# Performance work log

Measured on AMD Instinct MI355X. Metric: run time of the kernel, lower is better.

The kernel has to match this reference:

```python
import jax, jax.numpy as jnp
import numpy as np

B = 32768      # batch
D = 2          # input_dim
H = 2048       # hidden_dim
NQ = 4         # qubits


def setup_inputs() -> dict:
    key = jax.random.key(0)
    ks = jax.random.split(key, 14)

    def lin(k, fan_in, fan_out):
        # kaiming-uniform-ish init like nn.Linear
        bound = 1.0 / np.sqrt(fan_in)
        kw, kb = jax.random.split(k)
        W = jax.random.uniform(kw, (fan_in, fan_out), jnp.float32, -bound, bound)
        b = jax.random.uniform(kb, (fan_out,), jnp.float32, -bound, bound)
        return W, b

    x = jax.random.normal(ks[0], (B, D), jnp.float32)
    W1, b1 = lin(ks[1], D + NQ, H)      # core Linear 1
    W2, b2 = lin(ks[2], H, H)           # core Linear 2
    Wc, bc = lin(ks[3], H, 1)           # classifier
    Wr1, br1 = lin(ks[4], D, 8)
    Wr2, br2 = lin(ks[5], 8, 4)
    Wr3, br3 = lin(ks[6], 4, 1)
    return dict(x=x, W1=W1, b1=b1, W2=W2, b2=b2, Wc=Wc, bc=bc,
                Wr1=Wr1, br1=br1, Wr2=Wr2, br2=br2, Wr3=Wr3, br3=br3)


def _quantum_feature_map(x):
    # Exact closed form of: RY(x_i) on 4 qubits from |0000>, CNOT(0,1), CNOT(2,3),
    # expval(PauliZ(i)). Padding with zeros -> cos(0)=1 on unused wires.
    xq = jnp.pad(x, ((0, 0), (0, NQ - x.shape[1])))  # [B,4]
    c = jnp.cos(xq)
    return jnp.stack([c[:, 0], c[:, 0] * c[:, 1], c[:, 2], c[:, 2] * c[:, 3]], axis=1)


def reference(x, W1, b1, W2, b2, Wc, bc, Wr1, br1, Wr2, br2, Wr3, br3):
    qfeat = _quantum_feature_map(x)               # [B,4]
    concat = jnp.concatenate([x, qfeat], axis=1)  # [B, D+4]
    h = jnp.tanh(concat @ W1 + b1)                # [B,H]
    h = jnp.tanh(h @ W2 + b2)                     # [B,H]
    logits = h @ Wc + bc                          # [B,1]
    r = jnp.tanh(x @ Wr1 + br1)
    r = jnp.tanh(r @ Wr2 + br2)
    risk = r @ Wr3 + br3                          # [B,1]
    return logits, risk
```

## Files before the change

kernel.cpp:

```cpp
#include <hip/hip_runtime.h>
#include <hip/hip_bf16.h>
#include <stdint.h>

#define B_ROWS 32768
#define HID    2048
#define K_DIM  2048

#define BM 128
#define BN 256
#define BKB 128
#define NWIN (K_DIM / BKB)

#define SCALE_W   5747.3639f
#define DEQUANT   1.3700225e-6f

#define L1_BLOCKS (B_ROWS / 32)
#define TR_BLOCKS ((HID/32)*(K_DIM/32))

typedef int  int4v  __attribute__((ext_vector_type(4)));
typedef char char16 __attribute__((ext_vector_type(16)));

__device__ __forceinline__ float fast_tanh(float x) {
    float e = __expf(2.0f * x);
    return 1.0f - 2.0f * __builtin_amdgcn_rcpf(e + 1.0f);
}

__device__ __forceinline__ void gl_lds16(const void* g, void* l) {
    __builtin_amdgcn_global_load_lds(
        (const __attribute__((address_space(1))) void*)(uintptr_t)g,
        (__attribute__((address_space(3))) void*)(uint32_t)(uintptr_t)l,
        16, 0, 0);
}


__global__ __launch_bounds__(256) void prep_kernel(
    const float* __restrict__ x,   const float* __restrict__ W1, const float* __restrict__ b1,
    const float* __restrict__ W2,
    const float* __restrict__ Wr1, const float* __restrict__ br1,
    const float* __restrict__ Wr2, const float* __restrict__ br2,
    const float* __restrict__ Wr3, const float* __restrict__ br3,
    const float* __restrict__ bc,
    char* __restrict__ h1t, char* __restrict__ W2t, float* __restrict__ out) {
    const int t = threadIdx.x;
    if (blockIdx.x >= L1_BLOCKS) {
        __shared__ float tile[32][33];
        const int tb = blockIdx.x - L1_BLOCKS;
        const int n0 = (tb & 63) * 32;
        const int k0 = (tb >> 6) * 32;
        const int tx = t & 31;
        const int ty = t >> 5;
#pragma unroll
        for (int i = 0; i < 4; ++i) {
            int k = k0 + ty + i * 8;
            tile[ty + i * 8][tx] = W2[(size_t)k * HID + n0 + tx];
        }
        __syncthreads();
#pragma unroll
        for (int i = 0; i < 4; ++i) {
            int n = n0 + ty + i * 8;
            W2t[(size_t)n * K_DIM + k0 + tx] =
                (char)__float2int_rn(tile[tx][ty + i * 8] * SCALE_W);
        }
        return;
    }
    const int tx = t & 127;
    const int ty = t >> 7;
    const int n0 = tx * 16;
    float w0[16], w1[16], w2[16], w3[16], wb[16];
#pragma unroll
    for (int j = 0; j < 16; ++j) {
        w0[j] = W1[0 * HID + n0 + j];
        w1[j] = W1[1 * HID + n0 + j];
        w2[j] = W1[2 * HID + n0 + j];
        w3[j] = W1[3 * HID + n0 + j];
        wb[j] = W1[4 * HID + n0 + j] + W1[5 * HID + n0 + j] + b1[n0 + j];
    }
    const int brow0 = blockIdx.x * 32;
    char* base = h1t + (size_t)(brow0 >> 4) * 32768
               + (n0 >> 6) * 1024 + ((n0 >> 4) & 3) * 256;
    for (int r = ty; r < 32; r += 2) {
        const int b = brow0 + r;
        const float x0 = x[2 * b], x1 = x[2 * b + 1];
        const float c0 = cosf(x0);
        const float cc = c0 * cosf(x1);
        char16 v;
#pragma unroll
        for (int j = 0; j < 16; ++j) {
            float z = wb[j] + x0 * w0[j] + x1 * w1[j] + c0 * w2[j] + cc * w3[j];
            v[j] = (char)__float2int_rn(fast_tanh(z) * 127.0f);
        }
        *(char16*)(base + (r >> 4) * 32768 + (r & 15) * 16) = v;
    }
    if (t < 32) {
        const int b = brow0 + t;
        const float x0 = x[2 * b], x1 = x[2 * b + 1];
        float r1[8];
#pragma unroll
        for (int j = 0; j < 8; ++j)
            r1[j] = fast_tanh(br1[j] + x0 * Wr1[j] + x1 * Wr1[8 + j]);
        float r2[4];
#pragma unroll
        for (int j = 0; j < 4; ++j) {
            float s = br2[j];
#pragma unroll
            for (int i = 0; i < 8; ++i) s += r1[i] * Wr2[i * 4 + j];
            r2[j] = fast_tanh(s);
        }
        float risk = br3[0];
#pragma unroll
        for (int i = 0; i < 4; ++i) risk += r2[i] * Wr3[i];
        out[B_ROWS + b] = risk;
        out[b]          = bc[0];
    }
}

__global__ __launch_bounds__(256, 2) void gemm_kernel(
    const char* __restrict__ At,
    const char* __restrict__ Bt,
    const float* __restrict__ b2, const float* __restrict__ Wc,
    float* __restrict__ out) {
    __shared__ __align__(16) char sB[BN * BKB];

    const int tid  = threadIdx.x;
    const int wave = tid >> 6;
    const int lane = tid & 63;
    const int bid  = blockIdx.x;
    const int m0 = (bid >> 3) * BM;
    const int n0 = (bid & 7) * BN;

    const char* bSrc[8]; char* bDst[8];
    {
        const int rsub  = lane >> 3;
        const int chunk = (lane & 7) ^ rsub;
#pragma unroll
        for (int i = 0; i < 8; ++i) {
            int seg = wave * 8 + i;
            bSrc[i] = Bt + (size_t)(n0 + seg * 8 + rsub) * K_DIM + chunk * 16;
            bDst[i] = sB + seg * 1024;
        }
    }

    int4v acc[4][8] = {};
    const int mw   = (wave & 1) * 64;
    const int nw   = (wave >> 1) * 128;
    const int quad = lane >> 4;
    const int r16  = lane & 15;
    const int x7   = lane & 7;

    const char* aP[4];
#pragma unroll
    for (int mi = 0; mi < 4; ++mi)
        aP[mi] = At + (size_t)((m0 + mw) >> 4 << 15) + mi * 32768 + lane * 16;

    for (int w = 0; w < NWIN; ++w) {
#pragma unroll
        for (int i = 0; i < 8; ++i) {
            gl_lds16(bSrc[i], bDst[i]);
            bSrc[i] += BKB;
        }
        __syncthreads();
#pragma unroll
        for (int ks = 0; ks < 2; ++ks) {
            int4v af[4], bfr[8];
#pragma unroll
            for (int mi = 0; mi < 4; ++mi)
                af[mi] = *(const int4v*)(aP[mi] + ks * 1024);
            const int slot = ((ks * 4 + quad) ^ x7) * 16;
#pragma unroll
            for (int ni = 0; ni < 8; ++ni)
                bfr[ni] = *(const int4v*)(sB + (nw + ni * 16 + r16) * BKB + slot);
#pragma unroll
            for (int mi = 0; mi < 4; ++mi)
#pragma unroll
                for (int ni = 0; ni < 8; ++ni)
                    acc[mi][ni] = __builtin_amdgcn_mfma_i32_16x16x64_i8(
                        af[mi], bfr[ni], acc[mi][ni], 0, 0, 0);
        }
#pragma unroll
        for (int mi = 0; mi < 4; ++mi) aP[mi] += 2048;
        __syncthreads();
    }

    float b2v[8], wcv[8];
#pragma unroll
    for (int ni = 0; ni < 8; ++ni) {
        int gn = n0 + nw + ni * 16 + r16;
        b2v[ni] = b2[gn];
        wcv[ni] = Wc[gn];
    }
#pragma unroll
    for (int mi = 0; mi < 4; ++mi) {
#pragma unroll
        for (int r = 0; r < 4; ++r) {
            int gm = m0 + mw + mi * 16 + quad * 4 + r;
            float rs = 0.f;
#pragma unroll
            for (int ni = 0; ni < 8; ++ni)
                rs += fast_tanh((float)acc[mi][ni][r] * DEQUANT + b2v[ni]) * wcv[ni];
            rs += __shfl_xor(rs, 1);
            rs += __shfl_xor(rs, 2);
            rs += __shfl_xor(rs, 4);
            rs += __shfl_xor(rs, 8);
            if (r16 == 0) atomicAdd(&out[gm], rs);
        }
    }
}

extern "C" void kernel_launch(void* const* d_in, const int* in_sizes, int n_in,
                              void* d_out, int out_size, void* d_ws, size_t ws_size,
                              hipStream_t stream) {
    const float* x   = (const float*)d_in[0];
    const float* W1  = (const float*)d_in[1];
    const float* b1  = (const float*)d_in[2];
    const float* W2  = (const float*)d_in[3];
    const float* b2  = (const float*)d_in[4];
    const float* Wc  = (const float*)d_in[5];
    const float* bc  = (const float*)d_in[6];
    const float* Wr1 = (const float*)d_in[7];
    const float* br1 = (const float*)d_in[8];
    const float* Wr2 = (const float*)d_in[9];
    const float* br2 = (const float*)d_in[10];
    const float* Wr3 = (const float*)d_in[11];
    const float* br3 = (const float*)d_in[12];
    float* out = (float*)d_out;

    char* W2t = (char*)d_ws;
    char* h1t = (char*)d_ws + (size_t)4 * 1024 * 1024;

    prep_kernel<<<L1_BLOCKS + TR_BLOCKS, 256, 0, stream>>>(
        x, W1, b1, W2, Wr1, br1, Wr2, br2, Wr3, br3, bc, h1t, W2t, out);
    gemm_kernel<<<(B_ROWS / BM) * (HID / BN), 256, 0, stream>>>(h1t, W2t, b2, Wc, out);
}
```

Before: 299.6 us.

## Pre-swizzle W2 into MFMA fragment layout and load B directly from global

The prep kernel now writes the quantized W2 in the same per-16-row fragment-tiled layout already used for h1, so each lane's 16-byte MFMA operand is contiguous. The GEMM drops the LDS staging buffer, the async global-to-LDS copies and both barriers per K window, and instead loads both A and B fragments straight from global memory (L2/L1) every 64-wide K step. This removes LDS traffic and synchronization, and may raise occupancy. In exchange, B tiles are no longer shared through LDS across the waves of a block, so global/L2 load traffic increases, and there is no explicit prefetch to hide load latency.

```diff
diff --git a/kernel.cpp b/kernel.cpp
--- a/kernel.cpp
+++ b/kernel.cpp
@@ -8,8 +8,6 @@
 
 #define BM 128
 #define BN 256
-#define BKB 128
-#define NWIN (K_DIM / BKB)
 
 #define SCALE_W   5747.3639f
 #define DEQUANT   1.3700225e-6f
@@ -23,13 +21,6 @@
 __device__ __forceinline__ float fast_tanh(float x) {
     float e = __expf(2.0f * x);
     return 1.0f - 2.0f * __builtin_amdgcn_rcpf(e + 1.0f);
-}
-
-__device__ __forceinline__ void gl_lds16(const void* g, void* l) {
-    __builtin_amdgcn_global_load_lds(
-        (const __attribute__((address_space(1))) void*)(uintptr_t)g,
-        (__attribute__((address_space(3))) void*)(uint32_t)(uintptr_t)l,
-        16, 0, 0);
 }
 
 
@@ -40,7 +31,7 @@
     const float* __restrict__ Wr2, const float* __restrict__ br2,
     const float* __restrict__ Wr3, const float* __restrict__ br3,
     const float* __restrict__ bc,
-    char* __restrict__ h1t, char* __restrict__ W2t, float* __restrict__ out) {
+    char* __restrict__ h1t, char* __restrict__ W2tf, float* __restrict__ out) {
     const int t = threadIdx.x;
     if (blockIdx.x >= L1_BLOCKS) {
         __shared__ float tile[32][33];
@@ -55,11 +46,15 @@
             tile[ty + i * 8][tx] = W2[(size_t)k * HID + n0 + tx];
         }
         __syncthreads();
-#pragma unroll
-        for (int i = 0; i < 4; ++i) {
-            int n = n0 + ty + i * 8;
-            W2t[(size_t)n * K_DIM + k0 + tx] =
-                (char)__float2int_rn(tile[tx][ty + i * 8] * SCALE_W);
+        if (t < 64) {
+            const int n = n0 + (t & 31);
+            const int k = k0 + ((t >> 5) << 4);
+            char16 v;
+#pragma unroll
+            for (int j = 0; j < 16; ++j)
+                v[j] = (char)__float2int_rn(tile[(k - k0) + j][n - n0] * SCALE_W);
+            *(char16*)(W2tf + (size_t)(n >> 4) * 32768 + ((k >> 6) << 10)
+                       + (((k >> 4) & 3) << 8) + ((n & 15) << 4)) = v;
         }
         return;
     }
@@ -116,11 +111,9 @@
 
 __global__ __launch_bounds__(256, 2) void gemm_kernel(
     const char* __restrict__ At,
-    const char* __restrict__ Bt,
+    const char* __restrict__ Btf,
     const float* __restrict__ b2, const float* __restrict__ Wc,
     float* __restrict__ out) {
-    __shared__ __align__(16) char sB[BN * BKB];
-
     const int tid  = threadIdx.x;
     const int wave = tid >> 6;
     const int lane = tid & 63;
@@ -128,57 +121,38 @@
     const int m0 = (bid >> 3) * BM;
     const int n0 = (bid & 7) * BN;
 
-    const char* bSrc[8]; char* bDst[8];
-    {
-        const int rsub  = lane >> 3;
-        const int chunk = (lane & 7) ^ rsub;
-#pragma unroll
-        for (int i = 0; i < 8; ++i) {
-            int seg = wave * 8 + i;
-            bSrc[i] = Bt + (size_t)(n0 + seg * 8 + rsub) * K_DIM + chunk * 16;
-            bDst[i] = sB + seg * 1024;
-        }
-    }
-
-    int4v acc[4][8] = {};
     const int mw   = (wave & 1) * 64;
     const int nw   = (wave >> 1) * 128;
     const int quad = lane >> 4;
     const int r16  = lane & 15;
-    const int x7   = lane & 7;
-
-    const char* aP[4];
+
+    unsigned aOff[4], bOff[8];
 #pragma unroll
     for (int mi = 0; mi < 4; ++mi)
-        aP[mi] = At + (size_t)((m0 + mw) >> 4 << 15) + mi * 32768 + lane * 16;
-
-    for (int w = 0; w < NWIN; ++w) {
-#pragma unroll
-        for (int i = 0; i < 8; ++i) {
-            gl_lds16(bSrc[i], bDst[i]);
-            bSrc[i] += BKB;
-        }
-        __syncthreads();
-#pragma unroll
-        for (int ks = 0; ks < 2; ++ks) {
-            int4v af[4], bfr[8];
+        aOff[mi] = (unsigned)(((m0 + mw) >> 4) + mi) * 32768u + lane * 16;
+#pragma unroll
+    for (int ni = 0; ni < 8; ++ni)
+        bOff[ni] = (unsigned)(((n0 + nw) >> 4) + ni) * 32768u + lane * 16;
+
+    int4v acc[4][8] = {};
+    for (int k64 = 0; k64 < K_DIM / 64; ++k64) {
+        int4v af[4], bf[8];
+#pragma unroll
+        for (int mi = 0; mi < 4; ++mi) {
+            af[mi] = *(const int4v*)(At + aOff[mi]);
+            aOff[mi] += 1024;
+        }
+#pragma unroll
+        for (int ni = 0; ni < 8; ++ni) {
+            bf[ni] = *(const int4v*)(Btf + bOff[ni]);
+            bOff[ni] += 1024;
+        }
+#pragma unroll
+        for (int ni = 0; ni < 8; ++ni)
 #pragma unroll
             for (int mi = 0; mi < 4; ++mi)
-                af[mi] = *(const int4v*)(aP[mi] + ks * 1024);
-            const int slot = ((ks * 4 + quad) ^ x7) * 16;
-#pragma unroll
-            for (int ni = 0; ni < 8; ++ni)
-                bfr[ni] = *(const int4v*)(sB + (nw + ni * 16 + r16) * BKB + slot);
-#pragma unroll
-            for (int mi = 0; mi < 4; ++mi)
-#pragma unroll
-                for (int ni = 0; ni < 8; ++ni)
-                    acc[mi][ni] = __builtin_amdgcn_mfma_i32_16x16x64_i8(
-                        af[mi], bfr[ni], acc[mi][ni], 0, 0, 0);
-        }
-#pragma unroll
-        for (int mi = 0; mi < 4; ++mi) aP[mi] += 2048;
-        __syncthreads();
+                acc[mi][ni] = __builtin_amdgcn_mfma_i32_16x16x64_i8(
+                    af[mi], bf[ni], acc[mi][ni], 0, 0, 0);
     }
 
     float b2v[8], wcv[8];
@@ -224,10 +198,10 @@
     const float* br3 = (const float*)d_in[12];
     float* out = (float*)d_out;
 
-    char* W2t = (char*)d_ws;
-    char* h1t = (char*)d_ws + (size_t)4 * 1024 * 1024;
+    char* W2tf = (char*)d_ws;
+    char* h1t  = (char*)d_ws + (size_t)4 * 1024 * 1024;
 
     prep_kernel<<<L1_BLOCKS + TR_BLOCKS, 256, 0, stream>>>(
-        x, W1, b1, W2, Wr1, br1, Wr2, br2, Wr3, br3, bc, h1t, W2t, out);
-    gemm_kernel<<<(B_ROWS / BM) * (HID / BN), 256, 0, stream>>>(h1t, W2t, b2, Wc, out);
-}
+        x, W1, b1, W2, Wr1, br1, Wr2, br2, Wr3, br3, bc, h1t, W2tf, out);
+    gemm_kernel<<<(B_ROWS / BM) * (HID / BN), 256, 0, stream>>>(h1t, W2tf, b2, Wc, out);
+}
```

After: 287.6 us. 4.0% less time.
